# Kernel optimization log

Hardware: AMD Instinct MI355X
Metric: run time of the kernel (lower is better)

Reference implementation:

```python
import jax, jax.numpy as jnp
import numpy as np

B, N, H = 131072, 64, 8  # batch, n_agents (= n states = n coupling pins, ring), hidden width


def setup_inputs() -> dict:
    key = jax.random.key(0)
    ks = jax.random.split(key, 9)
    x = jax.random.normal(ks[0], (B, N), jnp.float32)
    # per-agent intrinsic MLP (heterogeneous agents, vectorized over agent dim)
    W1 = jax.random.normal(ks[1], (N, H), jnp.float32) * 0.5
    b1 = jax.random.normal(ks[2], (N, H), jnp.float32) * 0.1
    W2 = jax.random.normal(ks[3], (N, H), jnp.float32) * 0.5
    b2 = jax.random.normal(ks[4], (N,), jnp.float32) * 0.1
    # shared coupling MLP: takes [x_send, x_recv] -> scalar contribution
    Wc1 = jax.random.normal(ks[5], (2, H), jnp.float32) * 0.5
    bc1 = jax.random.normal(ks[6], (H,), jnp.float32) * 0.1
    Wc2 = jax.random.normal(ks[7], (H,), jnp.float32) * 0.5
    bc2 = jax.random.normal(ks[8], (1,), jnp.float32) * 0.1
    send_idx = jnp.arange(N, dtype=jnp.int32)
    recv_idx = (send_idx + 1) % N  # ring topology pins (send -> receive), symmetric coupling
    return dict(x=x, W1=W1, b1=b1, W2=W2, b2=b2, Wc1=Wc1, bc1=bc1,
                Wc2=Wc2, bc2=bc2, send_idx=send_idx, recv_idx=recv_idx)


def reference(x, W1, b1, W2, b2, Wc1, bc1, Wc2, bc2, send_idx, recv_idx):
    # ---- coupling_physics: gather pin features, shared MLP, symmetric scatter-add ----
    feats = jnp.stack([x[:, send_idx], x[:, recv_idx]], axis=-1)        # [B, E, 2]
    hc = jnp.tanh(jnp.einsum('bef,fh->beh', feats, Wc1) + bc1)          # [B, E, H]
    contrib = jnp.einsum('beh,h->be', hc, Wc2) + bc2                    # [B, E]
    interactions = (jnp.zeros_like(x)
                    .at[:, recv_idx].add(contrib)    # dx[:, receive] += contribution
                    .at[:, send_idx].add(-contrib))  # dx[:, send]    -= contribution (symmetric)
    # ---- intrinsic_physics: per-agent MLP on own state, plus aggregated interactions ----
    ha = jnp.tanh(x[..., None] * W1 + b1)                               # [B, N, H]
    dx = jnp.einsum('bnh,nh->bn', ha, W2) + b2 + interactions           # [B, N]
    return dx  # [:, :outsize] with outsize == N
```

## Files before the change

### kernel.cpp

```cpp
#include <hip/hip_runtime.h>

static constexpr int N_AGENTS = 64;
static constexpr int H_DIM    = 8;

__device__ __forceinline__ float fast_exp2(float v) {
#if __has_builtin(__builtin_amdgcn_exp2f)
    return __builtin_amdgcn_exp2f(v);
#else
    return exp2f(v);
#endif
}

__device__ __forceinline__ float fast_rcp(float v) {
#if __has_builtin(__builtin_amdgcn_rcpf)
    return __builtin_amdgcn_rcpf(v);
#else
    return 1.0f / v;
#endif
}


__global__ __launch_bounds__(256) void networked_ode_kernel(
    const float* __restrict__ x,
    const float* __restrict__ W1,
    const float* __restrict__ b1,
    const float* __restrict__ W2,
    const float* __restrict__ b2,
    const float* __restrict__ Wc1,
    const float* __restrict__ bc1,
    const float* __restrict__ Wc2,
    const float* __restrict__ bc2,
    const int* __restrict__ send_idx,
    const int* __restrict__ recv_idx,
    float* __restrict__ out,
    int B)
{
    const int lane           = threadIdx.x & 63;
    const int wave_in_block  = threadIdx.x >> 6;
    const int waves_per_blk  = blockDim.x >> 6;
    const int gwave          = blockIdx.x * waves_per_blk + wave_in_block;
    const int total_waves    = gridDim.x * waves_per_blk;

    const float K = 2.8853900817779268f;

    float w1s[H_DIM], b1s[H_DIM], m2w2[H_DIM];
    float acc0 = b2[lane];
#pragma unroll
    for (int h = 0; h < H_DIM; ++h) {
        w1s[h] = W1[lane * H_DIM + h] * K;
        b1s[h] = b1[lane * H_DIM + h] * K;
        const float w2v = W2[lane * H_DIM + h];
        m2w2[h] = -2.0f * w2v;
        acc0 += w2v;
    }

    float wcss[H_DIM], wcrs[H_DIM], bc1s[H_DIM], m2wc2[H_DIM];
    float c0 = bc2[0];
#pragma unroll
    for (int h = 0; h < H_DIM; ++h) {
        wcss[h] = Wc1[h] * K;
        wcrs[h] = Wc1[H_DIM + h] * K;
        bc1s[h] = bc1[h] * K;
        const float wc2v = Wc2[h];
        m2wc2[h] = -2.0f * wc2v;
        c0 += wc2v;
    }

    const int sidx = send_idx[lane];
    const int ridx = recv_idx[lane];

    __shared__ int inv_r_s[256], inv_s_s[256];
    const int base = wave_in_block * 64;
    inv_r_s[base + ridx] = lane;
    inv_s_s[base + sidx] = lane;
    __syncthreads();
    const int inv_r = inv_r_s[base + lane];
    const int inv_s = inv_s_s[base + lane];

    for (int row0 = gwave * 2; row0 < B; row0 += total_waves * 2) {
        const bool has1 = (row0 + 1) < B;

        float xv[2];
        xv[0] = x[(size_t)row0 * N_AGENTS + lane];
        xv[1] = has1 ? x[(size_t)(row0 + 1) * N_AGENTS + lane] : 0.0f;

        float xs[2], xr[2];
#pragma unroll
        for (int r = 0; r < 2; ++r) {
            xs[r] = __shfl(xv[r], sidx, 64);
            xr[r] = __shfl(xv[r], ridx, 64);
        }

        float c[2]   = {c0, c0};
        float acc[2] = {acc0, acc0};

#pragma unroll
        for (int h = 0; h < H_DIM; ++h) {
#pragma unroll
            for (int r = 0; r < 2; ++r) {
                const float a  = __builtin_fmaf(xs[r], wcss[h],
                                 __builtin_fmaf(xr[r], wcrs[h], bc1s[h]));
                const float rr = fast_rcp(fast_exp2(a) + 1.0f);
                c[r] = __builtin_fmaf(rr, m2wc2[h], c[r]);
            }
        }

#pragma unroll
        for (int h = 0; h < H_DIM; ++h) {
#pragma unroll
            for (int r = 0; r < 2; ++r) {
                const float a  = __builtin_fmaf(xv[r], w1s[h], b1s[h]);
                const float rr = fast_rcp(fast_exp2(a) + 1.0f);
                acc[r] = __builtin_fmaf(rr, m2w2[h], acc[r]);
            }
        }

#pragma unroll
        for (int r = 0; r < 2; ++r) {
            const float cr = __shfl(c[r], inv_r, 64);
            const float cs = __shfl(c[r], inv_s, 64);
            const float res = acc[r] + cr - cs;
            if (r == 0 || has1)
                out[(size_t)(row0 + r) * N_AGENTS + lane] = res;
        }
    }
}

extern "C" void kernel_launch(void* const* d_in, const int* in_sizes, int n_in,
                              void* d_out, int out_size, void* d_ws, size_t ws_size,
                              hipStream_t stream) {
    const float* x   = (const float*)d_in[0];
    const float* W1  = (const float*)d_in[1];
    const float* b1  = (const float*)d_in[2];
    const float* W2  = (const float*)d_in[3];
    const float* b2  = (const float*)d_in[4];
    const float* Wc1 = (const float*)d_in[5];
    const float* bc1 = (const float*)d_in[6];
    const float* Wc2 = (const float*)d_in[7];
    const float* bc2 = (const float*)d_in[8];
    const int* send_idx = (const int*)d_in[9];
    const int* recv_idx = (const int*)d_in[10];

    const int B = in_sizes[0] / N_AGENTS;

    const int blocks = 2048;
    networked_ode_kernel<<<blocks, dim3(256), 0, stream>>>(
        x, W1, b1, W2, b2, Wc1, bc1, Wc2, bc2, send_idx, recv_idx,
        (float*)d_out, B);
}
```

Baseline: 123.5 us.

## Process four rows per wave with packed v2f FMAs and skip identity send shuffles

Each wave now handles four rows per iteration instead of two, and the FMA arithmetic is packed into two-wide float vectors so the compiler can emit packed FP32 FMAs. A wave-uniform ballot detects when send_idx is the identity permutation and skips the corresponding shuffles in both the gather and the scatter step. This targets VALU instruction count and cross-lane traffic in a kernel dominated by transcendental math. In exchange it uses more registers per thread, which may lower occupancy, and leaves fewer loop iterations per wave.

```diff
diff --git a/kernel.cpp b/kernel.cpp
--- a/kernel.cpp
+++ b/kernel.cpp
@@ -1,7 +1,10 @@
 #include <hip/hip_runtime.h>
+
+typedef float v2f __attribute__((ext_vector_type(2)));
 
 static constexpr int N_AGENTS = 64;
 static constexpr int H_DIM    = 8;
+static constexpr int ROWS     = 4;
 
 __device__ __forceinline__ float fast_exp2(float v) {
 #if __has_builtin(__builtin_amdgcn_exp2f)
@@ -18,6 +21,11 @@
     return 1.0f / v;
 #endif
 }
+
+__device__ __forceinline__ v2f fma2(v2f a, v2f b, v2f c) {
+    return __builtin_elementwise_fma(a, b, c);
+}
+__device__ __forceinline__ v2f splat(float s) { return (v2f){s, s}; }
 
 
 __global__ __launch_bounds__(256) void networked_ode_kernel(
@@ -69,6 +77,8 @@
     const int sidx = send_idx[lane];
     const int ridx = recv_idx[lane];
 
+    const bool send_is_id = (__ballot(sidx == lane) == ~0ull);
+
     __shared__ int inv_r_s[256], inv_s_s[256];
     const int base = wave_in_block * 64;
     inv_r_s[base + ridx] = lane;
@@ -77,51 +87,68 @@
     const int inv_r = inv_r_s[base + lane];
     const int inv_s = inv_s_s[base + lane];
 
-    for (int row0 = gwave * 2; row0 < B; row0 += total_waves * 2) {
-        const bool has1 = (row0 + 1) < B;
-
-        float xv[2];
-        xv[0] = x[(size_t)row0 * N_AGENTS + lane];
-        xv[1] = has1 ? x[(size_t)(row0 + 1) * N_AGENTS + lane] : 0.0f;
-
-        float xs[2], xr[2];
+    for (int row0 = gwave * ROWS; row0 < B; row0 += total_waves * ROWS) {
+        float xv[ROWS], xs[ROWS], xr[ROWS];
 #pragma unroll
-        for (int r = 0; r < 2; ++r) {
-            xs[r] = __shfl(xv[r], sidx, 64);
-            xr[r] = __shfl(xv[r], ridx, 64);
+        for (int k = 0; k < ROWS; ++k) {
+            const int row = row0 + k;
+            xv[k] = (row < B) ? x[(size_t)row * N_AGENTS + lane] : 0.0f;
+        }
+#pragma unroll
+        for (int k = 0; k < ROWS; ++k) xr[k] = __shfl(xv[k], ridx, 64);
+        if (send_is_id) {
+#pragma unroll
+            for (int k = 0; k < ROWS; ++k) xs[k] = xv[k];
+        } else {
+#pragma unroll
+            for (int k = 0; k < ROWS; ++k) xs[k] = __shfl(xv[k], sidx, 64);
         }
 
-        float c[2]   = {c0, c0};
-        float acc[2] = {acc0, acc0};
+        v2f XV[2] = {{xv[0], xv[1]}, {xv[2], xv[3]}};
+        v2f XS[2] = {{xs[0], xs[1]}, {xs[2], xs[3]}};
+        v2f XR[2] = {{xr[0], xr[1]}, {xr[2], xr[3]}};
+        v2f C[2]  = {splat(c0), splat(c0)};
+        v2f A[2]  = {splat(acc0), splat(acc0)};
+        const v2f one = splat(1.0f);
 
 #pragma unroll
         for (int h = 0; h < H_DIM; ++h) {
+            const v2f wcs_ = splat(wcss[h]), wcr_ = splat(wcrs[h]);
+            const v2f bcs_ = splat(bc1s[h]), mwc_ = splat(m2wc2[h]);
 #pragma unroll
-            for (int r = 0; r < 2; ++r) {
-                const float a  = __builtin_fmaf(xs[r], wcss[h],
-                                 __builtin_fmaf(xr[r], wcrs[h], bc1s[h]));
-                const float rr = fast_rcp(fast_exp2(a) + 1.0f);
-                c[r] = __builtin_fmaf(rr, m2wc2[h], c[r]);
+            for (int p = 0; p < 2; ++p) {
+                v2f a = fma2(XR[p], wcr_, bcs_);
+                a = fma2(XS[p], wcs_, a);
+                v2f z; z.x = fast_exp2(a.x); z.y = fast_exp2(a.y);
+                z = z + one;
+                v2f r; r.x = fast_rcp(z.x); r.y = fast_rcp(z.y);
+                C[p] = fma2(r, mwc_, C[p]);
             }
         }
 
 #pragma unroll
         for (int h = 0; h < H_DIM; ++h) {
+            const v2f w1_ = splat(w1s[h]), b1_ = splat(b1s[h]);
+            const v2f mw2_ = splat(m2w2[h]);
 #pragma unroll
-            for (int r = 0; r < 2; ++r) {
-                const float a  = __builtin_fmaf(xv[r], w1s[h], b1s[h]);
-                const float rr = fast_rcp(fast_exp2(a) + 1.0f);
-                acc[r] = __builtin_fmaf(rr, m2w2[h], acc[r]);
+            for (int p = 0; p < 2; ++p) {
+                v2f a = fma2(XV[p], w1_, b1_);
+                v2f z; z.x = fast_exp2(a.x); z.y = fast_exp2(a.y);
+                z = z + one;
+                v2f r; r.x = fast_rcp(z.x); r.y = fast_rcp(z.y);
+                A[p] = fma2(r, mw2_, A[p]);
             }
         }
 
+        const float cv[ROWS] = {C[0].x, C[0].y, C[1].x, C[1].y};
+        const float av[ROWS] = {A[0].x, A[0].y, A[1].x, A[1].y};
 #pragma unroll
-        for (int r = 0; r < 2; ++r) {
-            const float cr = __shfl(c[r], inv_r, 64);
-            const float cs = __shfl(c[r], inv_s, 64);
-            const float res = acc[r] + cr - cs;
-            if (r == 0 || has1)
-                out[(size_t)(row0 + r) * N_AGENTS + lane] = res;
+        for (int k = 0; k < ROWS; ++k) {
+            const float cr = __shfl(cv[k], inv_r, 64);
+            const float cs = send_is_id ? cv[k] : __shfl(cv[k], inv_s, 64);
+            const int row = row0 + k;
+            if (row < B)
+                out[(size_t)row * N_AGENTS + lane] = av[k] + cr - cs;
         }
     }
 }
```

After: 121.3 us. Within noise of the previous version (-1.8%).
